# Kernel optimization log

Measured on AMD Instinct MI355X. Metric: run time of the kernel, lower is better.

The kernel has to match this reference:

```python
import jax, jax.numpy as jnp
import numpy as np

B, S, P, D = 128, 64, 32, 256   # batch, seq_len, pad_size, input_size
E, H, L, A, O = 256, 128, 2, 1, 2  # embed, hidden, n_layers, att_dim, output
INITRANGE = 0.1


def setup_inputs() -> dict:
    key = jax.random.key(0)
    ks = jax.random.split(key, 12)
    u = lambda k, shape: jax.random.uniform(k, shape, jnp.float32, -INITRANGE, INITRANGE)
    return {
        "inputs": jax.random.normal(ks[0], (B, S, P, D), jnp.float32),
        "conv_w": u(ks[1], (D,)),          # Conv1d(1,1,kernel=D) weight (output length is 1)
        "conv_b": u(ks[2], (1,)),
        "embed_w": u(ks[3], (E, D)),       # Linear(D,E,bias=False)
        "gru_Wih": u(ks[4], (L, 2, 3 * H, E)),  # [layer, direction, 3H, in] (E == 2H)
        "gru_Whh": u(ks[5], (L, 2, 3 * H, H)),
        "gru_bih": u(ks[6], (L, 2, 3 * H)),
        "gru_bhh": u(ks[7], (L, 2, 3 * H)),
        "att_w1": u(ks[8], (A, 2 * H)),    # Linear(2H, att_dim, bias=False)
        "lin_w": u(ks[9], (O, 2 * H)),
        "lin_b": u(ks[10], (O,)),
        "batch_size": B,
    }


def _gru_layer(x, Wih, Whh, bih, bhh, reverse):
    # x: [B,S,Din]; torch GRU cell semantics.
    xg = jnp.einsum('bsd,gd->sbg', x, Wih) + bih  # precompute input gates [S,B,3H]
    h0 = jnp.zeros((x.shape[0], Whh.shape[1]), x.dtype)

    def step(h, xg_t):
        gh = h @ Whh.T + bhh
        xr, xz, xn = jnp.split(xg_t, 3, axis=-1)
        hr, hz, hn = jnp.split(gh, 3, axis=-1)
        r = jax.nn.sigmoid(xr + hr)
        z = jax.nn.sigmoid(xz + hz)
        n = jnp.tanh(xn + r * hn)
        h_new = (1.0 - z) * n + z * h
        return h_new, h_new

    _, hs = jax.lax.scan(step, h0, xg, reverse=reverse)  # [S,B,H], time-aligned
    return jnp.swapaxes(hs, 0, 1)  # [B,S,H]


def _forward(inputs, conv_w, conv_b, embed_w, gru_Wih, gru_Whh, gru_bih, gru_bhh,
             att_w1, lin_w, lin_b, batch_size):
    # convolutional_layer: conv output length is 1 -> per-event scalar dot product,
    # then bmm gives a weighted sum of events within each visit.
    s = jnp.einsum('bspk,k->bsp', inputs, conv_w) + conv_b[0]      # [B,S,P]
    conv_all = jnp.einsum('bsp,bspk->bsk', s, inputs)               # [B,S,D]
    # embedding_layer: Linear(D,E) + Hardtanh
    x = jnp.clip(conv_all @ embed_w.T, -1.0, 1.0)                   # [B,S,E]
    # bidirectional multi-layer GRU, h0 = zeros (dropout_p = 0 -> identity)
    for l in range(L):
        f = _gru_layer(x, gru_Wih[l, 0], gru_Whh[l, 0], gru_bih[l, 0], gru_bhh[l, 0], False)
        b = _gru_layer(x, gru_Wih[l, 1], gru_Whh[l, 1], gru_bih[l, 1], gru_bhh[l, 1], True)
        x = jnp.concatenate([f, b], axis=-1)                        # [B,S,2H]
    states = x
    # add_attention: per-step Linear(2H, att_dim) + softmax over att_dim (nn.Softmax on [B,A])
    alpha = jax.nn.softmax(jnp.einsum('bsh,ah->bsa', states, att_w1), axis=-1)
    alpha = jnp.swapaxes(alpha, 1, 2)                               # [B,A,S]
    context = jnp.einsum('bas,bsh->bah', alpha, states).reshape(batch_size, -1)  # [B, A*2H]
    out = jax.nn.softmax(context @ lin_w.T + lin_b, axis=-1)        # [B,O]
    return out, states, context, alpha


def reference(inputs, conv_w, conv_b, embed_w, gru_Wih, gru_Whh, gru_bih, gru_bhh,
              att_w1, lin_w, lin_b, batch_size):
    return _forward(inputs, conv_w, conv_b, embed_w, gru_Wih, gru_Whh, gru_bih,
                    gru_bhh, att_w1, lin_w, lin_b, batch_size)
```

## Files before the change

kernel.cpp:

```cpp
#include <hip/hip_runtime.h>


using u16 = unsigned short;
using u32 = unsigned int;

typedef __bf16 bf16x8 __attribute__((ext_vector_type(8)));
typedef float  f32x4  __attribute__((ext_vector_type(4)));

__device__ __forceinline__ float bf2f(u16 u) {
  union { u32 i; float f; } v; v.i = ((u32)u) << 16; return v.f;
}
__device__ __forceinline__ u16 f2bf(float f) {
  union { float f; u32 i; } v; v.f = f;
  u32 i = v.i;
  u32 r = (i + 0x7FFFu + ((i >> 16) & 1u)) >> 16;
  return (u16)r;
}
__device__ __forceinline__ float sigm(float x) { return 1.f / (1.f + __expf(-x)); }
__device__ __forceinline__ float tanh_f(float x) { return 1.f - 2.f / (1.f + __expf(2.f * x)); }

__device__ __forceinline__ void split8(const float* v, bf16x8& hi, bf16x8& lo) {
  union { bf16x8 v; u16 s[8]; } H, L;
#pragma unroll
  for (int j = 0; j < 8; j++) {
    u16 h = f2bf(v[j]);
    H.s[j] = h;
    L.s[j] = f2bf(v[j] - bf2f(h));
  }
  hi = H.v; lo = L.v;
}

__global__ __launch_bounds__(256) void k_cvt(
    const float* __restrict__ embw, const float* __restrict__ Wih,
    u16* __restrict__ embHi, u16* __restrict__ embLo, u16* __restrict__ wihB) {
  const int i = blockIdx.x * 256 + threadIdx.x;
  if (i < 65536) {
    float v = embw[i];
    u16 h = f2bf(v);
    embHi[i] = h;
    embLo[i] = f2bf(v - bf2f(h));
  }
  wihB[i] = f2bf(Wih[i]);
}

__global__ __launch_bounds__(256) void k_conv(
    const float* __restrict__ inp, const float* __restrict__ cw,
    const float* __restrict__ cb, u16* __restrict__ chi, u16* __restrict__ clo) {
  __shared__ float tile[32 * 256];
  __shared__ float cwf[256];
  __shared__ float s_p[32];
  const int bs  = blockIdx.x;
  const int tid = threadIdx.x;
  const float* src = inp + (size_t)bs * 8192;
#pragma unroll
  for (int i = 0; i < 8; i++) {
    int idx = i * 1024 + tid * 4;
    *(float4*)&tile[idx] = *(const float4*)&src[idx];
  }
  cwf[tid] = cw[tid];
  __syncthreads();
  const int wv = tid >> 6, ln = tid & 63;
  const float cbf = cb[0];
  for (int pp = 0; pp < 8; pp++) {
    int p = wv * 8 + pp;
    float part = 0.f;
#pragma unroll
    for (int q = 0; q < 4; q++) {
      int k = ln + q * 64;
      part += tile[p * 256 + k] * cwf[k];
    }
    for (int off = 32; off; off >>= 1) part += __shfl_xor(part, off, 64);
    if (ln == 0) s_p[p] = part + cbf;
  }
  __syncthreads();
  float acc = 0.f;
  const int k = tid;
#pragma unroll
  for (int p = 0; p < 32; p++) acc += s_p[p] * tile[p * 256 + k];
  u16 hi = f2bf(acc);
  float lo = acc - bf2f(hi);
  chi[(size_t)bs * 256 + k] = hi;
  clo[(size_t)bs * 256 + k] = f2bf(lo);
}

template <bool HAS_ALO, bool HAS_WLO, bool HAS_BIAS, bool CLIP, bool OUT_BF16>
__global__ __launch_bounds__(256) void k_gemm(
    const u16* __restrict__ A, const u16* __restrict__ Alo,
    const u16* __restrict__ W, const u16* __restrict__ Wlo,
    const float* __restrict__ bias,
    void* __restrict__ Cout, int M, int N, int K) {
  const int LDT = 56;
  __shared__ u16 As[64 * 56];
  __shared__ u16 La[64 * 56];
  __shared__ u16 Ws[64 * 56];
  __shared__ u16 Lw[64 * 56];
  const int tid = threadIdx.x;
  const int m0 = blockIdx.x * 64, n0 = blockIdx.y * 64;
  const int wv = tid >> 6, ln = tid & 63;
  const int lm = ln & 15, lk = (ln >> 4) * 8;
  const int srow = tid >> 2, sgrp = tid & 3;

  f32x4 acc[4];
#pragma unroll
  for (int nt = 0; nt < 4; nt++) acc[nt] = (f32x4){0.f, 0.f, 0.f, 0.f};

  for (int kc = 0; kc < K; kc += 32) {
    __syncthreads();
    *(uint4*)&As[srow * LDT + sgrp * 8] =
        *(const uint4*)&A[(size_t)(m0 + srow) * K + kc + sgrp * 8];
    *(uint4*)&Ws[srow * LDT + sgrp * 8] =
        *(const uint4*)&W[(size_t)(n0 + srow) * K + kc + sgrp * 8];
    if (HAS_ALO)
      *(uint4*)&La[srow * LDT + sgrp * 8] =
          *(const uint4*)&Alo[(size_t)(m0 + srow) * K + kc + sgrp * 8];
    if (HAS_WLO)
      *(uint4*)&Lw[srow * LDT + sgrp * 8] =
          *(const uint4*)&Wlo[(size_t)(n0 + srow) * K + kc + sgrp * 8];
    __syncthreads();

    bf16x8 af = *(const bf16x8*)&As[(wv * 16 + lm) * LDT + lk];
    bf16x8 bfr[4];
#pragma unroll
    for (int nt = 0; nt < 4; nt++)
      bfr[nt] = *(const bf16x8*)&Ws[(nt * 16 + lm) * LDT + lk];
#pragma unroll
    for (int nt = 0; nt < 4; nt++)
      acc[nt] = __builtin_amdgcn_mfma_f32_16x16x32_bf16(af, bfr[nt], acc[nt], 0, 0, 0);
    if (HAS_ALO) {
      bf16x8 lf = *(const bf16x8*)&La[(wv * 16 + lm) * LDT + lk];
#pragma unroll
      for (int nt = 0; nt < 4; nt++)
        acc[nt] = __builtin_amdgcn_mfma_f32_16x16x32_bf16(lf, bfr[nt], acc[nt], 0, 0, 0);
    }
    if (HAS_WLO) {
#pragma unroll
      for (int nt = 0; nt < 4; nt++) {
        bf16x8 wl = *(const bf16x8*)&Lw[(nt * 16 + lm) * LDT + lk];
        acc[nt] = __builtin_amdgcn_mfma_f32_16x16x32_bf16(af, wl, acc[nt], 0, 0, 0);
      }
    }
  }

  const int rbase = m0 + wv * 16 + (ln >> 4) * 4;
#pragma unroll
  for (int nt = 0; nt < 4; nt++) {
    const int col = n0 + nt * 16 + lm;
    const float bv = HAS_BIAS ? bias[col] : 0.f;
#pragma unroll
    for (int r = 0; r < 4; r++) {
      float v = acc[nt][r] + bv;
      if (CLIP) v = fminf(fmaxf(v, -1.f), 1.f);
      const int row = rbase + r;
      if (OUT_BF16)
        ((u16*)Cout)[(size_t)row * N + col] = f2bf(v);
      else
        ((float*)Cout)[(size_t)row * N + col] = v;
    }
  }
}

__global__ __launch_bounds__(512, 2) void k_gru(
    const float* __restrict__ xg,
    const float* __restrict__ WhhL,
    const float* __restrict__ bhhL,
    u16* __restrict__ st_bf,
    float* __restrict__ st_f,
    float* __restrict__ ctx) {
  __shared__ __attribute__((aligned(16))) u16 hbHi[2][128];
  __shared__ __attribute__((aligned(16))) u16 hbLo[2][128];

  const int b   = blockIdx.x >> 1;
  const int dir = blockIdx.x & 1;
  const int tid = threadIdx.x;
  const int w   = tid >> 6, l = tid & 63;
  const int lm  = l & 15;
  const int kw  = (l >> 4) * 8;
  const int d   = w * 16 + lm;

  bf16x8 whi[3][4], wlo[3][4];
#pragma unroll
  for (int tt = 0; tt < 3; tt++) {
#pragma unroll
    for (int kt = 0; kt < 4; kt++) {
      const int row = (tt * 8 + w) * 16 + lm;
      const float* p = WhhL + ((size_t)(dir * 384 + row)) * 128 + kt * 32 + kw;
      float v[8];
      *(float4*)&v[0] = *(const float4*)&p[0];
      *(float4*)&v[4] = *(const float4*)&p[4];
      split8(v, whi[tt][kt], wlo[tt][kt]);
    }
  }
  float bhr = 0.f, bhz = 0.f, bhn = 0.f;
  if (l < 16) {
    bhr = bhhL[dir * 384 + d];
    bhz = bhhL[dir * 384 + 128 + d];
    bhn = bhhL[dir * 384 + 256 + d];
  }
  if (tid < 128) { hbHi[0][tid] = 0; hbLo[0][tid] = 0; }

  const float* xbase = xg + (size_t)(b * 64) * 768 + dir * 384 + d;
  float xr = 0.f, xz = 0.f, xn = 0.f;
  if (l < 16) {
    const int t0 = dir ? 63 : 0;
    xr = xbase[t0 * 768];
    xz = xbase[t0 * 768 + 128];
    xn = xbase[t0 * 768 + 256];
  }
  float hold = 0.f, csum = 0.f;
  __syncthreads();

  int cur = 0;
  for (int ti = 0; ti < 64; ti++) {
    const int t = dir ? (63 - ti) : ti;
    float nxr = 0.f, nxz = 0.f, nxn = 0.f;
    if (l < 16 && ti < 63) {
      const int tn = dir ? (62 - ti) : (ti + 1);
      nxr = xbase[tn * 768];
      nxz = xbase[tn * 768 + 128];
      nxn = xbase[tn * 768 + 256];
    }
    bf16x8 ahi[4], alo[4];
#pragma unroll
    for (int kt = 0; kt < 4; kt++) {
      ahi[kt] = *(const bf16x8*)&hbHi[cur][kt * 32 + kw];
      alo[kt] = *(const bf16x8*)&hbLo[cur][kt * 32 + kw];
    }
    f32x4 acc[3];
#pragma unroll
    for (int tt = 0; tt < 3; tt++) acc[tt] = (f32x4){0.f, 0.f, 0.f, 0.f};
#pragma unroll
    for (int kt = 0; kt < 4; kt++) {
#pragma unroll
      for (int tt = 0; tt < 3; tt++) {
        acc[tt] = __builtin_amdgcn_mfma_f32_16x16x32_bf16(ahi[kt], whi[tt][kt], acc[tt], 0, 0, 0);
        acc[tt] = __builtin_amdgcn_mfma_f32_16x16x32_bf16(alo[kt], whi[tt][kt], acc[tt], 0, 0, 0);
        acc[tt] = __builtin_amdgcn_mfma_f32_16x16x32_bf16(ahi[kt], wlo[tt][kt], acc[tt], 0, 0, 0);
      }
    }
    const int nxt = cur ^ 1;
    if (l < 16) {
      const float rg = sigm(xr + bhr + acc[0][0]);
      const float zg = sigm(xz + bhz + acc[1][0]);
      const float ng = tanh_f(xn + rg * (acc[2][0] + bhn));
      const float hn = (1.f - zg) * ng + zg * hold;
      hold = hn;
      csum += hn;
      const u16 hh = f2bf(hn);
      hbHi[nxt][d] = hh;
      hbLo[nxt][d] = f2bf(hn - bf2f(hh));
      const size_t oi = (size_t)(b * 64 + t) * 256 + dir * 128 + d;
      if (st_bf) st_bf[oi] = hh;
      if (st_f)  st_f[oi]  = hn;
    }
    __syncthreads();
    cur = nxt;
    xr = nxr; xz = nxz; xn = nxn;
  }
  if (ctx != nullptr && l < 16)
    ctx[(size_t)b * 256 + dir * 128 + d] = csum;
}

__global__ __launch_bounds__(256) void k_final(
    const float* __restrict__ ctx, const float* __restrict__ lw,
    const float* __restrict__ lb, float* __restrict__ out,
    float* __restrict__ alpha) {
  const int tid = threadIdx.x;
  if (tid < 128) {
    const int b = tid;
    float a0 = lb[0], a1 = lb[1];
    for (int k = 0; k < 256; k++) {
      float c = ctx[b * 256 + k];
      a0 += c * lw[k];
      a1 += c * lw[256 + k];
    }
    float m = fmaxf(a0, a1);
    float e0 = __expf(a0 - m), e1 = __expf(a1 - m);
    float s = e0 + e1;
    out[2 * b]     = e0 / s;
    out[2 * b + 1] = e1 / s;
  }
  for (int i = tid; i < 8192; i += 256) alpha[i] = 1.0f;
}

extern "C" void kernel_launch(void* const* d_in, const int* in_sizes, int n_in,
                              void* d_out, int out_size, void* d_ws, size_t ws_size,
                              hipStream_t stream) {
  const float* inp   = (const float*)d_in[0];
  const float* convw = (const float*)d_in[1];
  const float* convb = (const float*)d_in[2];
  const float* embw  = (const float*)d_in[3];
  const float* Wih   = (const float*)d_in[4];
  const float* Whh   = (const float*)d_in[5];
  const float* bih   = (const float*)d_in[6];
  const float* bhh   = (const float*)d_in[7];
  const float* lw    = (const float*)d_in[9];
  const float* lb    = (const float*)d_in[10];

  char* ws = (char*)d_ws;
  u16*   convHi = (u16*)(ws);
  u16*   convLo = (u16*)(ws + 4194304u);
  u16*   xbuf   = (u16*)(ws + 8388608u);
  u16*   embHi  = (u16*)(ws + 12582912u);
  u16*   embLo  = (u16*)(ws + 12713984u);
  u16*   wihB   = (u16*)(ws + 12845056u);
  float* xgbuf  = (float*)(ws + 13631488u);
  u16*   states0 = convHi;

  float* outp    = (float*)d_out;
  float* statesO = outp + 256;
  float* ctxO    = outp + 2097408;
  float* alphaO  = outp + 2130176;

  k_cvt<<<1536, 256, 0, stream>>>(embw, Wih, embHi, embLo, wihB);

  k_conv<<<8192, 256, 0, stream>>>(inp, convw, convb, convHi, convLo);

  dim3 gE(128, 4);
  k_gemm<true, true, false, true, true><<<gE, 256, 0, stream>>>(
      convHi, convLo, embHi, embLo, nullptr, xbuf, 8192, 256, 256);

  dim3 gX(128, 12);
  k_gemm<false, false, true, false, false><<<gX, 256, 0, stream>>>(
      xbuf, nullptr, wihB, nullptr, bih, xgbuf, 8192, 768, 256);

  k_gru<<<256, 512, 0, stream>>>(xgbuf, Whh, bhh, states0, nullptr, nullptr);

  k_gemm<false, false, true, false, false><<<gX, 256, 0, stream>>>(
      states0, nullptr, wihB + 196608, nullptr, bih + 768, xgbuf, 8192, 768, 256);

  k_gru<<<256, 512, 0, stream>>>(xgbuf, Whh + 98304, bhh + 768,
                                 nullptr, statesO, ctxO);

  k_final<<<1, 256, 0, stream>>>(ctxO, lw, lb, outp, alphaO);
}
```

Measured before the change: 564.9 us.

## Use fp16 split-precision MFMA in GRU recurrence, lighter barrier, parallel final head

The GRU recurrent matmul moves from bf16 hi/lo splitting with three MFMAs per tile to fp16 hi/lo splitting with two MFMAs. Odd lanes load the low half of h and even lanes the high half, and the two partial sums from each accumulator are added together. The per-step __syncthreads is replaced by an explicit lgkmcnt wait plus s_barrier. The final linear/softmax kernel now runs on 128 blocks with wave shuffle reductions instead of one serial block. The aim is to shorten the serial per-step MFMA chain, at some precision risk from fp16 range and a subtler reduction layout.

```diff
diff --git a/kernel.cpp b/kernel.cpp
--- a/kernel.cpp
+++ b/kernel.cpp
@@ -4,8 +4,9 @@
 using u16 = unsigned short;
 using u32 = unsigned int;
 
-typedef __bf16 bf16x8 __attribute__((ext_vector_type(8)));
-typedef float  f32x4  __attribute__((ext_vector_type(4)));
+typedef __bf16    bf16x8 __attribute__((ext_vector_type(8)));
+typedef _Float16  f16x8  __attribute__((ext_vector_type(8)));
+typedef float     f32x4  __attribute__((ext_vector_type(4)));
 
 __device__ __forceinline__ float bf2f(u16 u) {
   union { u32 i; float f; } v; v.i = ((u32)u) << 16; return v.f;
@@ -18,17 +19,6 @@
 }
 __device__ __forceinline__ float sigm(float x) { return 1.f / (1.f + __expf(-x)); }
 __device__ __forceinline__ float tanh_f(float x) { return 1.f - 2.f / (1.f + __expf(2.f * x)); }
-
-__device__ __forceinline__ void split8(const float* v, bf16x8& hi, bf16x8& lo) {
-  union { bf16x8 v; u16 s[8]; } H, L;
-#pragma unroll
-  for (int j = 0; j < 8; j++) {
-    u16 h = f2bf(v[j]);
-    H.s[j] = h;
-    L.s[j] = f2bf(v[j] - bf2f(h));
-  }
-  hi = H.v; lo = L.v;
-}
 
 __global__ __launch_bounds__(256) void k_cvt(
     const float* __restrict__ embw, const float* __restrict__ Wih,
@@ -166,8 +156,8 @@
     u16* __restrict__ st_bf,
     float* __restrict__ st_f,
     float* __restrict__ ctx) {
-  __shared__ __attribute__((aligned(16))) u16 hbHi[2][128];
-  __shared__ __attribute__((aligned(16))) u16 hbLo[2][128];
+  __shared__ __attribute__((aligned(16))) _Float16 hbHi[2][128];
+  __shared__ __attribute__((aligned(16))) _Float16 hbLo[2][128];
 
   const int b   = blockIdx.x >> 1;
   const int dir = blockIdx.x & 1;
@@ -177,17 +167,23 @@
   const int kw  = (l >> 4) * 8;
   const int d   = w * 16 + lm;
 
-  bf16x8 whi[3][4], wlo[3][4];
+  f16x8 whi[3][4], wlo[3][4];
 #pragma unroll
   for (int tt = 0; tt < 3; tt++) {
 #pragma unroll
     for (int kt = 0; kt < 4; kt++) {
       const int row = (tt * 8 + w) * 16 + lm;
       const float* p = WhhL + ((size_t)(dir * 384 + row)) * 128 + kt * 32 + kw;
-      float v[8];
-      *(float4*)&v[0] = *(const float4*)&p[0];
-      *(float4*)&v[4] = *(const float4*)&p[4];
-      split8(v, whi[tt][kt], wlo[tt][kt]);
+      union { f16x8 v; _Float16 s[8]; } Wh, Wl;
+#pragma unroll
+      for (int j = 0; j < 8; j++) {
+        float v = p[j];
+        _Float16 h = (_Float16)v;
+        Wh.s[j] = h;
+        Wl.s[j] = (_Float16)(v - (float)h);
+      }
+      whi[tt][kt] = Wh.v;
+      wlo[tt][kt] = Wl.v;
     }
   }
   float bhr = 0.f, bhz = 0.f, bhn = 0.f;
@@ -196,7 +192,7 @@
     bhz = bhhL[dir * 384 + 128 + d];
     bhn = bhhL[dir * 384 + 256 + d];
   }
-  if (tid < 128) { hbHi[0][tid] = 0; hbLo[0][tid] = 0; }
+  if (tid < 128) { hbHi[0][tid] = (_Float16)0.f; hbLo[0][tid] = (_Float16)0.f; }
 
   const float* xbase = xg + (size_t)(b * 64) * 768 + dir * 384 + d;
   float xr = 0.f, xz = 0.f, xn = 0.f;
@@ -219,40 +215,46 @@
       nxz = xbase[tn * 768 + 128];
       nxn = xbase[tn * 768 + 256];
     }
-    bf16x8 ahi[4], alo[4];
+    const _Float16* hsrc = (l & 1) ? hbLo[cur] : hbHi[cur];
+    f16x8 af[4];
+#pragma unroll
+    for (int kt = 0; kt < 4; kt++)
+      af[kt] = *(const f16x8*)&hsrc[kt * 32 + kw];
+
+    f32x4 aH[3], aL[3];
+#pragma unroll
+    for (int tt = 0; tt < 3; tt++) {
+      aH[tt] = (f32x4){0.f, 0.f, 0.f, 0.f};
+      aL[tt] = (f32x4){0.f, 0.f, 0.f, 0.f};
+    }
 #pragma unroll
     for (int kt = 0; kt < 4; kt++) {
-      ahi[kt] = *(const bf16x8*)&hbHi[cur][kt * 32 + kw];
-      alo[kt] = *(const bf16x8*)&hbLo[cur][kt * 32 + kw];
-    }
-    f32x4 acc[3];
-#pragma unroll
-    for (int tt = 0; tt < 3; tt++) acc[tt] = (f32x4){0.f, 0.f, 0.f, 0.f};
-#pragma unroll
-    for (int kt = 0; kt < 4; kt++) {
 #pragma unroll
       for (int tt = 0; tt < 3; tt++) {
-        acc[tt] = __builtin_amdgcn_mfma_f32_16x16x32_bf16(ahi[kt], whi[tt][kt], acc[tt], 0, 0, 0);
-        acc[tt] = __builtin_amdgcn_mfma_f32_16x16x32_bf16(alo[kt], whi[tt][kt], acc[tt], 0, 0, 0);
-        acc[tt] = __builtin_amdgcn_mfma_f32_16x16x32_bf16(ahi[kt], wlo[tt][kt], acc[tt], 0, 0, 0);
+        aH[tt] = __builtin_amdgcn_mfma_f32_16x16x32_f16(af[kt], whi[tt][kt], aH[tt], 0, 0, 0);
+        aL[tt] = __builtin_amdgcn_mfma_f32_16x16x32_f16(af[kt], wlo[tt][kt], aL[tt], 0, 0, 0);
       }
     }
     const int nxt = cur ^ 1;
     if (l < 16) {
-      const float rg = sigm(xr + bhr + acc[0][0]);
-      const float zg = sigm(xz + bhz + acc[1][0]);
-      const float ng = tanh_f(xn + rg * (acc[2][0] + bhn));
+      const float ghr = aH[0][0] + aH[0][1] + aL[0][0] + aL[0][1];
+      const float ghz = aH[1][0] + aH[1][1] + aL[1][0] + aL[1][1];
+      const float ghn = aH[2][0] + aH[2][1] + aL[2][0] + aL[2][1];
+      const float rg = sigm(xr + bhr + ghr);
+      const float zg = sigm(xz + bhz + ghz);
+      const float ng = tanh_f(xn + rg * (ghn + bhn));
       const float hn = (1.f - zg) * ng + zg * hold;
       hold = hn;
       csum += hn;
-      const u16 hh = f2bf(hn);
+      const _Float16 hh = (_Float16)hn;
       hbHi[nxt][d] = hh;
-      hbLo[nxt][d] = f2bf(hn - bf2f(hh));
+      hbLo[nxt][d] = (_Float16)(hn - (float)hh);
       const size_t oi = (size_t)(b * 64 + t) * 256 + dir * 128 + d;
-      if (st_bf) st_bf[oi] = hh;
+      if (st_bf) st_bf[oi] = f2bf(hn);
       if (st_f)  st_f[oi]  = hn;
     }
-    __syncthreads();
+    asm volatile("s_waitcnt lgkmcnt(0)" ::: "memory");
+    __builtin_amdgcn_s_barrier();
     cur = nxt;
     xr = nxr; xz = nxz; xn = nxn;
   }
@@ -260,26 +262,34 @@
     ctx[(size_t)b * 256 + dir * 128 + d] = csum;
 }
 
-__global__ __launch_bounds__(256) void k_final(
+__global__ __launch_bounds__(64) void k_final(
     const float* __restrict__ ctx, const float* __restrict__ lw,
     const float* __restrict__ lb, float* __restrict__ out,
     float* __restrict__ alpha) {
-  const int tid = threadIdx.x;
-  if (tid < 128) {
-    const int b = tid;
-    float a0 = lb[0], a1 = lb[1];
-    for (int k = 0; k < 256; k++) {
-      float c = ctx[b * 256 + k];
-      a0 += c * lw[k];
-      a1 += c * lw[256 + k];
-    }
-    float m = fmaxf(a0, a1);
-    float e0 = __expf(a0 - m), e1 = __expf(a1 - m);
-    float s = e0 + e1;
+  const int b = blockIdx.x;
+  const int l = threadIdx.x;
+  float a0 = 0.f, a1 = 0.f;
+#pragma unroll
+  for (int q = 0; q < 4; q++) {
+    const int k = q * 64 + l;
+    const float c = ctx[b * 256 + k];
+    a0 += c * lw[k];
+    a1 += c * lw[256 + k];
+  }
+  for (int off = 32; off; off >>= 1) {
+    a0 += __shfl_xor(a0, off, 64);
+    a1 += __shfl_xor(a1, off, 64);
+  }
+  alpha[b * 64 + l] = 1.0f;
+  if (l == 0) {
+    a0 += lb[0];
+    a1 += lb[1];
+    const float m = fmaxf(a0, a1);
+    const float e0 = __expf(a0 - m), e1 = __expf(a1 - m);
+    const float s = e0 + e1;
     out[2 * b]     = e0 / s;
     out[2 * b + 1] = e1 / s;
   }
-  for (int i = tid; i < 8192; i += 256) alpha[i] = 1.0f;
 }
 
 extern "C" void kernel_launch(void* const* d_in, const int* in_sizes, int n_in,
@@ -331,5 +341,5 @@
   k_gru<<<256, 512, 0, stream>>>(xgbuf, Whh + 98304, bhh + 768,
                                  nullptr, statesO, ctxO);
 
-  k_final<<<1, 256, 0, stream>>>(ctxO, lw, lb, outp, alphaO);
-}
+  k_final<<<128, 64, 0, stream>>>(ctxO, lw, lb, outp, alphaO);
+}
```

Result: faster. 536.8 us (-5.0%).
